# Performance work log

Hardware: AMD Instinct MI355X
Metric: run time of the kernel (lower is better)

The kernel has to match this reference:

```python
import jax, jax.numpy as jnp
import numpy as np

N = 131072      # total nodes = num_graphs * numNodes
E = 2097152     # edges (avg degree 16)
C_IN = 64
HID = 64        # hiddenChannels
NODES = 128     # numNodes per graph
B = 1024        # num_graphs
NCLS = 4


def setup_inputs() -> dict:
    key = jax.random.key(0)
    ks = jax.random.split(key, 10)
    x = jax.random.normal(ks[0], (N, C_IN), jnp.float32)
    edge_index = jax.random.randint(ks[1], (2, E), 0, N, dtype=jnp.int32)
    edge_attr = jax.random.uniform(ks[2], (E,), jnp.float32)
    # GCNConv params (stored as [in, out]); PyG uses glorot init, bias zeros
    W1 = jax.random.normal(ks[3], (C_IN, 2 * HID), jnp.float32) * (1.0 / np.sqrt(C_IN))
    b1 = jnp.zeros((2 * HID,), jnp.float32)
    W2 = jax.random.normal(ks[4], (2 * HID, HID), jnp.float32) * (1.0 / np.sqrt(2 * HID))
    b2 = jnp.zeros((HID,), jnp.float32)
    Wfc = jax.random.normal(ks[5], (HID * NODES, NCLS), jnp.float32) * (1.0 / np.sqrt(HID * NODES))
    bfc = jnp.zeros((NCLS,), jnp.float32)
    return {"x": x, "edge_index": edge_index, "edge_attr": edge_attr,
            "W1": W1, "b1": b1, "W2": W2, "b2": b2, "Wfc": Wfc, "bfc": bfc}


def gcn_conv(x, src, dst, ew, W, b):
    # PyG GCNConv: add self-loops (weight 1), symmetric normalization,
    # linear transform, scatter-add aggregation at target nodes, + bias.
    loop = jnp.arange(N, dtype=src.dtype)
    s = jnp.concatenate([src, loop])
    d = jnp.concatenate([dst, loop])
    w = jnp.concatenate([ew, jnp.ones((N,), ew.dtype)])
    deg = jax.ops.segment_sum(w, d, num_segments=N)                  # [N]
    dis = jnp.where(deg > 0, jax.lax.rsqrt(jnp.maximum(deg, 1e-30)), 0.0)
    norm = dis[s] * w * dis[d]                                       # [E+N]
    h = x @ W                                                        # [N, out]
    msg = h[s] * norm[:, None]                                       # gather + scale
    out = jax.ops.segment_sum(msg, d, num_segments=N)                # scatter-add
    return out + b


def reference(x, edge_index, edge_attr, W1, b1, W2, b2, Wfc, bfc):
    src, dst = edge_index[0], edge_index[1]
    h = jax.nn.relu(gcn_conv(x, src, dst, edge_attr, W1, b1))
    h = jax.nn.relu(gcn_conv(h, src, dst, edge_attr, W2, b2))
    h = h.reshape(B, HID * NODES)
    logits = h @ Wfc + bfc
    return jax.nn.softmax(logits, axis=1)
```

## Files before the change

kernel.cpp:

```cpp
#include <hip/hip_runtime.h>

#define N_NODES 131072
#define NE      2097152
#define CIN     64
#define HID     64
#define H2X     128
#define NODESG  128
#define NGRAPH  1024
#define NCLS    4

#define NBUCK   256
#define NPB     512
#define HBLK    1024
#define EPB     2048
#define DEGSC   1048576.0f
#define DEGMASK ((1ull << 40) - 1)

typedef short bf16x8 __attribute__((ext_vector_type(8)));
typedef float f32x4  __attribute__((ext_vector_type(4)));

__device__ __forceinline__ unsigned short f2b(float f) {
    unsigned int u = __float_as_uint(f);
    return (unsigned short)((u + 0x7fffu + ((u >> 16) & 1u)) >> 16);
}
__device__ __forceinline__ unsigned int pack2(float a, float b) {
    return (unsigned int)f2b(a) | ((unsigned int)f2b(b) << 16);
}
__device__ __forceinline__ float blo(unsigned u) { return __uint_as_float(u << 16); }
__device__ __forceinline__ float bhi(unsigned u) { return __uint_as_float(u & 0xffff0000u); }


__global__ __launch_bounds__(256) void k_wswiz(
        const float* __restrict__ W1, const float* __restrict__ W2,
        unsigned short* __restrict__ wf1, unsigned short* __restrict__ wf2) {
    int tid = threadIdx.x;
    #pragma unroll
    for (int it = 0; it < 4; ++it) {
        int idx = tid + 256 * it;
        int kt = idx >> 9, nt = (idx >> 6) & 7, l = idx & 63;
        int lm = l & 15, lq = l >> 4;
        unsigned pk[4];
        #pragma unroll
        for (int jp = 0; jp < 4; ++jp) {
            float w0 = W1[(kt*32 + lq*8 + 2*jp)     * H2X + nt*16 + lm];
            float w1 = W1[(kt*32 + lq*8 + 2*jp + 1) * H2X + nt*16 + lm];
            pk[jp] = pack2(w0, w1);
        }
        *(uint4*)&wf1[idx * 8] = make_uint4(pk[0], pk[1], pk[2], pk[3]);
    }
    #pragma unroll
    for (int it = 0; it < 4; ++it) {
        int idx = tid + 256 * it;
        int kt = idx >> 8, nt = (idx >> 6) & 3, l = idx & 63;
        int lm = l & 15, lq = l >> 4;
        unsigned pk[4];
        #pragma unroll
        for (int jp = 0; jp < 4; ++jp) {
            float w0 = W2[(kt*32 + lq*8 + 2*jp)     * HID + nt*16 + lm];
            float w1 = W2[(kt*32 + lq*8 + 2*jp + 1) * HID + nt*16 + lm];
            pk[jp] = pack2(w0, w1);
        }
        *(uint4*)&wf2[idx * 8] = make_uint4(pk[0], pk[1], pk[2], pk[3]);
    }
}


__global__ __launch_bounds__(256) void k_hist(const int* __restrict__ dst,
                                              int* __restrict__ hist) {
    __shared__ unsigned bh[NBUCK];
    int t = threadIdx.x;
    bh[t] = 0;
    __syncthreads();
    int base = blockIdx.x * EPB;
    #pragma unroll
    for (int k = 0; k < EPB / 256; ++k) {
        int d = dst[base + t + 256 * k];
        atomicAdd(&bh[d >> 9], 1u);
    }
    __syncthreads();
    hist[t * HBLK + blockIdx.x] = (int)bh[t];
}

__global__ void k_scan1(const int* __restrict__ in, int* __restrict__ out,
                        int* __restrict__ partial) {
    __shared__ int sd[256];
    int t = threadIdx.x;
    int base = blockIdx.x * 512;
    int c0 = in[base + 2*t];
    int c1 = in[base + 2*t + 1];
    int loc = c0 + c1;
    sd[t] = loc;
    __syncthreads();
    for (int off = 1; off < 256; off <<= 1) {
        int v = (t >= off) ? sd[t - off] : 0;
        __syncthreads();
        sd[t] += v;
        __syncthreads();
    }
    int excl = sd[t] - loc;
    out[base + 2*t]     = excl;
    out[base + 2*t + 1] = excl + c0;
    if (t == 255) partial[blockIdx.x] = sd[t];
}

__global__ void k_scan2(int* __restrict__ partial) {
    __shared__ int sd[256];
    int t = threadIdx.x;
    int p0 = partial[2*t], p1 = partial[2*t + 1];
    int loc = p0 + p1;
    sd[t] = loc;
    __syncthreads();
    for (int off = 1; off < 256; off <<= 1) {
        int v = (t >= off) ? sd[t - off] : 0;
        __syncthreads();
        sd[t] += v;
        __syncthreads();
    }
    int excl = sd[t] - loc;
    partial[2*t]     = excl;
    partial[2*t + 1] = excl + p0;
}

__global__ __launch_bounds__(256) void k_scatter(
        const int* __restrict__ src, const int* __restrict__ dst,
        const float* __restrict__ ew, const int* __restrict__ hist,
        const int* __restrict__ partial, unsigned long long* __restrict__ part) {
    __shared__ unsigned lcur[NBUCK];
    int t = threadIdx.x;
    int gi = t * HBLK + blockIdx.x;
    lcur[t] = (unsigned)(hist[gi] + partial[gi >> 9]);
    __syncthreads();
    int base = blockIdx.x * EPB;
    #pragma unroll
    for (int k = 0; k < EPB / 256; ++k) {
        int e = base + t + 256 * k;
        int s = src[e], d = dst[e];
        unsigned w = __float_as_uint(ew[e]);
        unsigned p = atomicAdd(&lcur[d >> 9], 1u);
        part[p] = ((unsigned long long)w << 32) |
                  ((unsigned long long)(unsigned)(d & 511) << 17) |
                  (unsigned long long)(unsigned)s;
    }
}

__global__ __launch_bounds__(256) void k_bucket(
        const unsigned long long* __restrict__ part, const int* __restrict__ hist,
        const int* __restrict__ partial, int2* __restrict__ csr,
        int* __restrict__ rowptr, int* __restrict__ counts, float* __restrict__ dis) {
    __shared__ unsigned long long dc[NPB];
    __shared__ unsigned cnt2[NPB];
    __shared__ int rp[NPB];
    __shared__ int sd[256];
    int t = threadIdx.x, b = blockIdx.x;
    dc[t] = 0; dc[t + 256] = 0;
    cnt2[t] = 0; cnt2[t + 256] = 0;
    __syncthreads();
    int start = hist[b * HBLK] + partial[2 * b];
    int end   = (b == NBUCK - 1) ? NE : (hist[(b + 1) * HBLK] + partial[2 * (b + 1)]);

    for (int j = start + t; j < end; j += 256) {
        unsigned long long p = part[j];
        unsigned dl = (unsigned)(p >> 17) & 511u;
        float w = __uint_as_float((unsigned)(p >> 32));
        atomicAdd(&dc[dl], (1ull << 40) | (unsigned long long)(unsigned)(w * DEGSC));
    }
    __syncthreads();

    unsigned long long d0 = dc[2*t], d1 = dc[2*t + 1];
    int c0 = (int)(d0 >> 40), c1 = (int)(d1 >> 40);
    int loc = c0 + c1;
    sd[t] = loc;
    __syncthreads();
    for (int off = 1; off < 256; off <<= 1) {
        int v = (t >= off) ? sd[t - off] : 0;
        __syncthreads();
        sd[t] += v;
        __syncthreads();
    }
    int excl = sd[t] - loc;
    rp[2*t] = excl; rp[2*t + 1] = excl + c0;

    int n0 = b * NPB;
    rowptr[n0 + 2*t]     = start + excl;
    rowptr[n0 + 2*t + 1] = start + excl + c0;
    counts[n0 + 2*t]     = c0;
    counts[n0 + 2*t + 1] = c1;
    float dg0 = (float)(d0 & DEGMASK) * (1.0f / DEGSC);
    float dg1 = (float)(d1 & DEGMASK) * (1.0f / DEGSC);
    dis[n0 + 2*t]     = rsqrtf(dg0 + 1.0f);
    dis[n0 + 2*t + 1] = rsqrtf(dg1 + 1.0f);
    __syncthreads();

    for (int j = start + t; j < end; j += 256) {
        unsigned long long p = part[j];
        unsigned dl = (unsigned)(p >> 17) & 511u;
        int s = (int)(p & 0x1ffffu);
        unsigned r = atomicAdd(&cnt2[dl], 1u);
        csr[start + rp[dl] + (int)r] = make_int2(s, (int)(unsigned)(p >> 32));
    }
}

__global__ void k_xcast(const float* __restrict__ x, const float* __restrict__ dis,
                        uint2* __restrict__ xb2) {
    int i = blockIdx.x * blockDim.x + threadIdx.x;
    float d = dis[i >> 4];
    float4 v = ((const float4*)x)[i];
    xb2[i] = make_uint2(pack2(d * v.x, d * v.y), pack2(d * v.z, d * v.w));
}


#define GATHER_PAIR(TAB, pA, pB, nA, nB, cmA, cmB, a0,a1,a2,a3, b0,b1,b2,b3, vSA, vSB) \
    {                                                                                  \
        int   sA0 = __shfl(pA.x, qid),      sA1 = __shfl(pA.x, qid + 4);               \
        int   sA2 = __shfl(pA.x, qid + 8),  sA3 = __shfl(pA.x, qid + 12);              \
        float fA0 = __int_as_float(__shfl(pA.y, qid));                                 \
        float fA1 = __int_as_float(__shfl(pA.y, qid + 4));                             \
        float fA2 = __int_as_float(__shfl(pA.y, qid + 8));                             \
        float fA3 = __int_as_float(__shfl(pA.y, qid + 12));                            \
        int   sB0 = __shfl(pB.x, qid),      sB1 = __shfl(pB.x, qid + 4);               \
        int   sB2 = __shfl(pB.x, qid + 8),  sB3 = __shfl(pB.x, qid + 12);              \
        float fB0 = __int_as_float(__shfl(pB.y, qid));                                 \
        float fB1 = __int_as_float(__shfl(pB.y, qid + 4));                             \
        float fB2 = __int_as_float(__shfl(pB.y, qid + 8));                             \
        float fB3 = __int_as_float(__shfl(pB.y, qid + 12));                            \
        uint2 vA0 = TAB[((unsigned)sA0 << 4) | ql];                                    \
        uint2 vA1 = TAB[((unsigned)sA1 << 4) | ql];                                    \
        uint2 vA2 = TAB[((unsigned)sA2 << 4) | ql];                                    \
        uint2 vA3 = TAB[((unsigned)sA3 << 4) | ql];                                    \
        uint2 vB0 = TAB[((unsigned)sB0 << 4) | ql];                                    \
        uint2 vB1 = TAB[((unsigned)sB1 << 4) | ql];                                    \
        uint2 vB2 = TAB[((unsigned)sB2 << 4) | ql];                                    \
        uint2 vB3 = TAB[((unsigned)sB3 << 4) | ql];                                    \
        vSA = TAB[((unsigned)nA << 4) | ql];                                           \
        vSB = TAB[((unsigned)nB << 4) | ql];                                           \
        a0 = fmaf(fA0, blo(vA0.x), a0); a1 = fmaf(fA0, bhi(vA0.x), a1);                \
        a2 = fmaf(fA0, blo(vA0.y), a2); a3 = fmaf(fA0, bhi(vA0.y), a3);                \
        a0 = fmaf(fA1, blo(vA1.x), a0); a1 = fmaf(fA1, bhi(vA1.x), a1);                \
        a2 = fmaf(fA1, blo(vA1.y), a2); a3 = fmaf(fA1, bhi(vA1.y), a3);                \
        a0 = fmaf(fA2, blo(vA2.x), a0); a1 = fmaf(fA2, bhi(vA2.x), a1);                \
        a2 = fmaf(fA2, blo(vA2.y), a2); a3 = fmaf(fA2, bhi(vA2.y), a3);                \
        a0 = fmaf(fA3, blo(vA3.x), a0); a1 = fmaf(fA3, bhi(vA3.x), a1);                \
        a2 = fmaf(fA3, blo(vA3.y), a2); a3 = fmaf(fA3, bhi(vA3.y), a3);                \
        b0 = fmaf(fB0, blo(vB0.x), b0); b1 = fmaf(fB0, bhi(vB0.x), b1);                \
        b2 = fmaf(fB0, blo(vB0.y), b2); b3 = fmaf(fB0, bhi(vB0.y), b3);                \
        b0 = fmaf(fB1, blo(vB1.x), b0); b1 = fmaf(fB1, bhi(vB1.x), b1);                \
        b2 = fmaf(fB1, blo(vB1.y), b2); b3 = fmaf(fB1, bhi(vB1.y), b3);                \
        b0 = fmaf(fB2, blo(vB2.x), b0); b1 = fmaf(fB2, bhi(vB2.x), b1);                \
        b2 = fmaf(fB2, blo(vB2.y), b2); b3 = fmaf(fB2, bhi(vB2.y), b3);                \
        b0 = fmaf(fB3, blo(vB3.x), b0); b1 = fmaf(fB3, bhi(vB3.x), b1);                \
        b2 = fmaf(fB3, blo(vB3.y), b2); b3 = fmaf(fB3, bhi(vB3.y), b3);                \
        int tsA = (cmA > 16) ? ((cmA - 13) >> 2) : 0;                                  \
        for (int k = 0; k < tsA; ++k) {                                                \
            int jj = 16 + 4 * k + qid;                                                 \
            int   s = __shfl(pA.x, jj);                                                \
            float f = __int_as_float(__shfl(pA.y, jj));                                \
            uint2 v = TAB[((unsigned)s << 4) | ql];                                    \
            a0 = fmaf(f, blo(v.x), a0); a1 = fmaf(f, bhi(v.x), a1);                    \
            a2 = fmaf(f, blo(v.y), a2); a3 = fmaf(f, bhi(v.y), a3);                    \
        }                                                                              \
        int tsB = (cmB > 16) ? ((cmB - 13) >> 2) : 0;                                  \
        for (int k = 0; k < tsB; ++k) {                                                \
            int jj = 16 + 4 * k + qid;                                                 \
            int   s = __shfl(pB.x, jj);                                                \
            float f = __int_as_float(__shfl(pB.y, jj));                                \
            uint2 v = TAB[((unsigned)s << 4) | ql];                                    \
            b0 = fmaf(f, blo(v.x), b0); b1 = fmaf(f, bhi(v.x), b1);                    \
            b2 = fmaf(f, blo(v.y), b2); b3 = fmaf(f, bhi(v.y), b3);                    \
        }                                                                              \
        a0 += __shfl_xor(a0, 16); a1 += __shfl_xor(a1, 16);                            \
        a2 += __shfl_xor(a2, 16); a3 += __shfl_xor(a3, 16);                            \
        a0 += __shfl_xor(a0, 32); a1 += __shfl_xor(a1, 32);                            \
        a2 += __shfl_xor(a2, 32); a3 += __shfl_xor(a3, 32);                            \
        b0 += __shfl_xor(b0, 16); b1 += __shfl_xor(b1, 16);                            \
        b2 += __shfl_xor(b2, 16); b3 += __shfl_xor(b3, 16);                            \
        b0 += __shfl_xor(b0, 32); b1 += __shfl_xor(b1, 32);                            \
        b2 += __shfl_xor(b2, 32); b3 += __shfl_xor(b3, 32);                            \
    }


__global__ __launch_bounds__(256, 4) void k_layer1(
        const uint2* __restrict__ xb2, const int2* __restrict__ csr,
        const int* __restrict__ rowptr, const int* __restrict__ counts,
        const float* __restrict__ dis, const unsigned short* __restrict__ wf1,
        const unsigned short* __restrict__ wf2, const float* __restrict__ b1,
        unsigned short* __restrict__ t2u) {
    __shared__ unsigned short sagg_b[32][72];
    __shared__ unsigned short sh1[32][136];
    __shared__ float sb[H2X];
    int tid = threadIdx.x;
    if (tid < H2X) sb[tid] = b1[tid];

    int wave = tid >> 6, lane = tid & 63;
    int qid = lane >> 4, ql = lane & 15;
    int n0 = blockIdx.x * 32;
    int nb = n0 + wave * 8;

    int cm8[8], cnt8[8], rs8[8];
    float dn8[8];
    int2 myp[8];
    #pragma unroll
    for (int i = 0; i < 8; ++i) {
        rs8[i] = rowptr[nb + i];
        cnt8[i] = counts[nb + i];
        dn8[i] = dis[nb + i];
        cm8[i] = cnt8[i] < 64 ? cnt8[i] : 64;
    }
    #pragma unroll
    for (int i = 0; i < 8; ++i)
        myp[i] = (lane < cm8[i]) ? csr[rs8[i] + lane] : make_int2(0, 0);

    #pragma unroll
    for (int ip = 0; ip < 8; ip += 2) {
        int2 pA = myp[ip], pB = myp[ip + 1];
        int nA = nb + ip, nB = nA + 1;
        float a0 = 0.f, a1 = 0.f, a2 = 0.f, a3 = 0.f;
        float b0 = 0.f, b1v = 0.f, b2v = 0.f, b3 = 0.f;
        uint2 vSA, vSB;
        GATHER_PAIR(xb2, pA, pB, nA, nB, cm8[ip], cm8[ip + 1],
                    a0, a1, a2, a3, b0, b1v, b2v, b3, vSA, vSB);
        for (int jj = 64; jj < cnt8[ip]; ++jj) {
            int2 p = csr[rs8[ip] + jj];
            float f = __int_as_float(p.y);
            uint2 v = xb2[((unsigned)p.x << 4) | ql];
            if (qid == 0) {
                a0 += f * blo(v.x); a1 += f * bhi(v.x);
                a2 += f * blo(v.y); a3 += f * bhi(v.y);
            }
        }
        for (int jj = 64; jj < cnt8[ip + 1]; ++jj) {
            int2 p = csr[rs8[ip + 1] + jj];
            float f = __int_as_float(p.y);
            uint2 v = xb2[((unsigned)p.x << 4) | ql];
            if (qid == 0) {
                b0 += f * blo(v.x); b1v += f * bhi(v.x);
                b2v += f * blo(v.y); b3 += f * bhi(v.y);
            }
        }
        if (qid == 0) {
            float dnA = dn8[ip], dnB = dn8[ip + 1];
            int m = wave * 8 + ip;
            *(uint2*)&sagg_b[m][ql * 4] =
                make_uint2(pack2(dnA * (a0 + blo(vSA.x)), dnA * (a1 + bhi(vSA.x))),
                           pack2(dnA * (a2 + blo(vSA.y)), dnA * (a3 + bhi(vSA.y))));
            *(uint2*)&sagg_b[m + 1][ql * 4] =
                make_uint2(pack2(dnB * (b0 + blo(vSB.x)), dnB * (b1v + bhi(vSB.x))),
                           pack2(dnB * (b2v + blo(vSB.y)), dnB * (b3 + bhi(vSB.y))));
        }
    }
    __syncthreads();

    int mt = wave & 1, ntb = (wave >> 1) * 4;
    int lm = lane & 15, lq = lane >> 4;
    bf16x8 af0 = *(const bf16x8*)&sagg_b[mt*16 + lm][lq * 8];
    bf16x8 af1 = *(const bf16x8*)&sagg_b[mt*16 + lm][32 + lq * 8];
    #pragma unroll
    for (int t = 0; t < 4; ++t) {
        int nt = ntb + t;
        bf16x8 bf0 = *(const bf16x8*)&wf1[(nt*64 + lane) * 8];
        bf16x8 bf1 = *(const bf16x8*)&wf1[((8 + nt)*64 + lane) * 8];
        f32x4 acc = {0.f, 0.f, 0.f, 0.f};
        acc = __builtin_amdgcn_mfma_f32_16x16x32_bf16(af0, bf0, acc, 0, 0, 0);
        acc = __builtin_amdgcn_mfma_f32_16x16x32_bf16(af1, bf1, acc, 0, 0, 0);
        int ch = nt*16 + lm;
        float bias = sb[ch];
        #pragma unroll
        for (int r = 0; r < 4; ++r)
            sh1[mt*16 + lq*4 + r][ch] = f2b(fmaxf(acc[r] + bias, 0.f));
    }
    __syncthreads();

    #pragma unroll
    for (int ti = 0; ti < 2; ++ti) {
        int t = wave * 2 + ti;
        int mt2 = t & 1, nt2 = t >> 1;
        f32x4 acc = {0.f, 0.f, 0.f, 0.f};
        #pragma unroll
        for (int kt = 0; kt < 4; ++kt) {
            bf16x8 af = *(const bf16x8*)&sh1[mt2*16 + lm][kt*32 + lq*8];
            bf16x8 bf = *(const bf16x8*)&wf2[((kt*4 + nt2)*64 + lane) * 8];
            acc = __builtin_amdgcn_mfma_f32_16x16x32_bf16(af, bf, acc, 0, 0, 0);
        }
        int ch = nt2*16 + lm;
        #pragma unroll
        for (int r = 0; r < 4; ++r) {
            int node = n0 + mt2*16 + lq*4 + r;
            t2u[(size_t)node * HID + ch] = f2b(dis[node] * acc[r]);
        }
    }
}


__global__ __launch_bounds__(256, 4) void k_agg2(
        const uint2* __restrict__ t2y, const int2* __restrict__ csr,
        const int* __restrict__ rowptr, const int* __restrict__ counts,
        const float* __restrict__ dis, const float* __restrict__ b2,
        unsigned short* __restrict__ h2b) {
    int tid = threadIdx.x;
    int wave = tid >> 6, lane = tid & 63;
    int qid = lane >> 4, ql = lane & 15;
    float4 bb = *(const float4*)&b2[ql * 4];
    int n0 = blockIdx.x * 32;
    int nb = n0 + wave * 8;

    int cm8[8], cnt8[8], rs8[8];
    float dn8[8];
    int2 myp[8];
    #pragma unroll
    for (int i = 0; i < 8; ++i) {
        rs8[i] = rowptr[nb + i];
        cnt8[i] = counts[nb + i];
        dn8[i] = dis[nb + i];
        cm8[i] = cnt8[i] < 64 ? cnt8[i] : 64;
    }
    #pragma unroll
    for (int i = 0; i < 8; ++i)
        myp[i] = (lane < cm8[i]) ? csr[rs8[i] + lane] : make_int2(0, 0);

    #pragma unroll
    for (int ip = 0; ip < 8; ip += 2) {
        int2 pA = myp[ip], pB = myp[ip + 1];
        int nA = nb + ip, nB = nA + 1;
        float a0 = 0.f, a1 = 0.f, a2 = 0.f, a3 = 0.f;
        float b0 = 0.f, b1v = 0.f, b2v = 0.f, b3 = 0.f;
        uint2 vSA, vSB;
        GATHER_PAIR(t2y, pA, pB, nA, nB, cm8[ip], cm8[ip + 1],
                    a0, a1, a2, a3, b0, b1v, b2v, b3, vSA, vSB);
        for (int jj = 64; jj < cnt8[ip]; ++jj) {
            int2 p = csr[rs8[ip] + jj];
            float f = __int_as_float(p.y);
            uint2 v = t2y[((unsigned)p.x << 4) | ql];
            if (qid == 0) {
                a0 += f * blo(v.x); a1 += f * bhi(v.x);
                a2 += f * blo(v.y); a3 += f * bhi(v.y);
            }
        }
        for (int jj = 64; jj < cnt8[ip + 1]; ++jj) {
            int2 p = csr[rs8[ip + 1] + jj];
            float f = __int_as_float(p.y);
            uint2 v = t2y[((unsigned)p.x << 4) | ql];
            if (qid == 0) {
                b0 += f * blo(v.x); b1v += f * bhi(v.x);
                b2v += f * blo(v.y); b3 += f * bhi(v.y);
            }
        }
        if (qid == 0) {
            float dnA = dn8[ip], dnB = dn8[ip + 1];
            float oa0 = fmaxf(fmaf(dnA, a0 + blo(vSA.x), bb.x), 0.f);
            float oa1 = fmaxf(fmaf(dnA, a1 + bhi(vSA.x), bb.y), 0.f);
            float oa2 = fmaxf(fmaf(dnA, a2 + blo(vSA.y), bb.z), 0.f);
            float oa3 = fmaxf(fmaf(dnA, a3 + bhi(vSA.y), bb.w), 0.f);
            float ob0 = fmaxf(fmaf(dnB, b0 + blo(vSB.x), bb.x), 0.f);
            float ob1 = fmaxf(fmaf(dnB, b1v + bhi(vSB.x), bb.y), 0.f);
            float ob2 = fmaxf(fmaf(dnB, b2v + blo(vSB.y), bb.z), 0.f);
            float ob3 = fmaxf(fmaf(dnB, b3 + bhi(vSB.y), bb.w), 0.f);
            *(uint2*)&h2b[((unsigned)nA << 6) | (ql * 4)] =
                make_uint2(pack2(oa0, oa1), pack2(oa2, oa3));
            *(uint2*)&h2b[((unsigned)nB << 6) | (ql * 4)] =
                make_uint2(pack2(ob0, ob1), pack2(ob2, ob3));
        }
    }
}


__global__ __launch_bounds__(256) void k_fc(
        const unsigned short* __restrict__ h2b, const float* __restrict__ Wfc,
        const float* __restrict__ bfc, float* __restrict__ out) {
    __shared__ float4 red[256];
    int b = blockIdx.x, t = threadIdx.x;
    const uint2* hrow = (const uint2*)(h2b + (size_t)b * (HID * NODESG));
    const float4* W4 = (const float4*)Wfc;
    float4 a = make_float4(0.f, 0.f, 0.f, 0.f);
    #pragma unroll
    for (int j = 0; j < 8; ++j) {
        int i = j * 256 + t;
        uint2 hv = hrow[i];
        float h0 = blo(hv.x), h1 = bhi(hv.x), h2v = blo(hv.y), h3 = bhi(hv.y);
        float4 w0 = W4[i * 4 + 0];
        float4 w1 = W4[i * 4 + 1];
        float4 w2 = W4[i * 4 + 2];
        float4 w3 = W4[i * 4 + 3];
        a.x = fmaf(h0, w0.x, a.x); a.y = fmaf(h0, w0.y, a.y);
        a.z = fmaf(h0, w0.z, a.z); a.w = fmaf(h0, w0.w, a.w);
        a.x = fmaf(h1, w1.x, a.x); a.y = fmaf(h1, w1.y, a.y);
        a.z = fmaf(h1, w1.z, a.z); a.w = fmaf(h1, w1.w, a.w);
        a.x = fmaf(h2v, w2.x, a.x); a.y = fmaf(h2v, w2.y, a.y);
        a.z = fmaf(h2v, w2.z, a.z); a.w = fmaf(h2v, w2.w, a.w);
        a.x = fmaf(h3, w3.x, a.x); a.y = fmaf(h3, w3.y, a.y);
        a.z = fmaf(h3, w3.z, a.z); a.w = fmaf(h3, w3.w, a.w);
    }
    red[t] = a;
    __syncthreads();
    for (int s = 128; s > 0; s >>= 1) {
        if (t < s) {
            red[t].x += red[t + s].x; red[t].y += red[t + s].y;
            red[t].z += red[t + s].z; red[t].w += red[t + s].w;
        }
        __syncthreads();
    }
    if (t == 0) {
        float l0 = red[0].x + bfc[0];
        float l1 = red[0].y + bfc[1];
        float l2 = red[0].z + bfc[2];
        float l3 = red[0].w + bfc[3];
        float mx = fmaxf(fmaxf(l0, l1), fmaxf(l2, l3));
        float e0 = expf(l0 - mx), e1 = expf(l1 - mx);
        float e2 = expf(l2 - mx), e3 = expf(l3 - mx);
        float inv = 1.f / (e0 + e1 + e2 + e3);
        float4 o = make_float4(e0 * inv, e1 * inv, e2 * inv, e3 * inv);
        *(float4*)&out[(size_t)b * 4] = o;
    }
}


extern "C" void kernel_launch(void* const* d_in, const int* in_sizes, int n_in,
                              void* d_out, int out_size, void* d_ws, size_t ws_size,
                              hipStream_t stream) {
    const float* x   = (const float*)d_in[0];
    const int*   ei  = (const int*)  d_in[1];
    const float* ea  = (const float*)d_in[2];
    const float* W1  = (const float*)d_in[3];
    const float* b1  = (const float*)d_in[4];
    const float* W2  = (const float*)d_in[5];
    const float* b2  = (const float*)d_in[6];
    const float* Wfc = (const float*)d_in[7];
    const float* bfc = (const float*)d_in[8];
    float* out = (float*)d_out;
    const int* src = ei;
    const int* dst = ei + NE;

    char* ws = (char*)d_ws;
    size_t off = 0;
    int*   hist   = (int*)  (ws + off); off += (size_t)NBUCK * HBLK * 4;
    int*   partial= (int*)  (ws + off); off += 4096;
    int*   counts = (int*)  (ws + off); off += (size_t)N_NODES * 4;
    int*   rowptr = (int*)  (ws + off); off += (size_t)N_NODES * 4;
    float* dis    = (float*)(ws + off); off += (size_t)N_NODES * 4;
    unsigned short* wf1 = (unsigned short*)(ws + off); off += 8192 * 2;
    unsigned short* wf2 = (unsigned short*)(ws + off); off += 8192 * 2;
    int2*  csr    = (int2*) (ws + off); off += (size_t)NE * 8;
    uint2* xb2    = (uint2*)(ws + off); off += (size_t)N_NODES * CIN * 2;
    unsigned short* t2u = (unsigned short*)(ws + off); off += (size_t)N_NODES * HID * 2;
    unsigned short* h2b = (unsigned short*)(ws + off); off += (size_t)N_NODES * HID * 2;
    unsigned long long* part = (unsigned long long*)t2u;

    hipMemsetAsync(hist, 0, (size_t)NBUCK * HBLK * 4 + 4096, stream);

    k_wswiz  <<<1, 256, 0, stream>>>(W1, W2, wf1, wf2);
    k_hist   <<<HBLK, 256, 0, stream>>>(dst, hist);
    k_scan1  <<<NBUCK * HBLK / 512, 256, 0, stream>>>(hist, hist, partial);
    k_scan2  <<<1, 256, 0, stream>>>(partial);
    k_scatter<<<HBLK, 256, 0, stream>>>(src, dst, ea, hist, partial, part);
    k_bucket <<<NBUCK, 256, 0, stream>>>(part, hist, partial, csr, rowptr, counts, dis);
    k_xcast  <<<(N_NODES * CIN / 4) / 256, 256, 0, stream>>>(x, dis, xb2);
    k_layer1 <<<N_NODES / 32, 256, 0, stream>>>(xb2, csr, rowptr, counts, dis,
                                                wf1, wf2, b1, t2u);
    k_agg2   <<<N_NODES / 32, 256, 0, stream>>>((const uint2*)t2u, csr, rowptr,
                                                counts, dis, b2, h2b);
    k_fc     <<<NGRAPH, 256, 0, stream>>>(h2b, Wfc, bfc, out);
}
```

Baseline: 264.2 us.

## Use 1024 finer buckets in CSR build, parallelize weight swizzle, drop memset

The counting-sort CSR construction now uses 1024 buckets of 128 nodes instead of 256 buckets of 512 nodes. This gives the bucket kernel four times as many blocks with smaller shared-memory work, and the histogram, scatter and scan kernels are adapted to match. The weight swizzle runs on 8 blocks instead of one, and the workspace memset is removed because every hist entry is written anyway. In exchange the histogram and scan arrays grow four times larger, and the per-block scans inside the bucket kernel leave most threads idle.

```diff
diff --git a/kernel.cpp b/kernel.cpp
--- a/kernel.cpp
+++ b/kernel.cpp
@@ -9,8 +9,8 @@
 #define NGRAPH  1024
 #define NCLS    4
 
-#define NBUCK   256
-#define NPB     512
+#define NBUCK   1024
+#define NPB     128
 #define HBLK    1024
 #define EPB     2048
 #define DEGSC   1048576.0f
@@ -33,10 +33,8 @@
 __global__ __launch_bounds__(256) void k_wswiz(
         const float* __restrict__ W1, const float* __restrict__ W2,
         unsigned short* __restrict__ wf1, unsigned short* __restrict__ wf2) {
-    int tid = threadIdx.x;
-    #pragma unroll
-    for (int it = 0; it < 4; ++it) {
-        int idx = tid + 256 * it;
+    int idx = blockIdx.x * 256 + threadIdx.x;
+    if (idx < 1024) {
         int kt = idx >> 9, nt = (idx >> 6) & 7, l = idx & 63;
         int lm = l & 15, lq = l >> 4;
         unsigned pk[4];
@@ -47,11 +45,9 @@
             pk[jp] = pack2(w0, w1);
         }
         *(uint4*)&wf1[idx * 8] = make_uint4(pk[0], pk[1], pk[2], pk[3]);
-    }
-    #pragma unroll
-    for (int it = 0; it < 4; ++it) {
-        int idx = tid + 256 * it;
-        int kt = idx >> 8, nt = (idx >> 6) & 3, l = idx & 63;
+    } else {
+        int j = idx - 1024;
+        int kt = j >> 8, nt = (j >> 6) & 3, l = j & 63;
         int lm = l & 15, lq = l >> 4;
         unsigned pk[4];
         #pragma unroll
@@ -60,7 +56,7 @@
             float w1 = W2[(kt*32 + lq*8 + 2*jp + 1) * HID + nt*16 + lm];
             pk[jp] = pack2(w0, w1);
         }
-        *(uint4*)&wf2[idx * 8] = make_uint4(pk[0], pk[1], pk[2], pk[3]);
+        *(uint4*)&wf2[j * 8] = make_uint4(pk[0], pk[1], pk[2], pk[3]);
     }
 }
 
@@ -69,16 +65,21 @@
                                               int* __restrict__ hist) {
     __shared__ unsigned bh[NBUCK];
     int t = threadIdx.x;
-    bh[t] = 0;
+    #pragma unroll
+    for (int k = 0; k < NBUCK / 256; ++k) bh[t + 256 * k] = 0;
     __syncthreads();
     int base = blockIdx.x * EPB;
     #pragma unroll
     for (int k = 0; k < EPB / 256; ++k) {
         int d = dst[base + t + 256 * k];
-        atomicAdd(&bh[d >> 9], 1u);
-    }
-    __syncthreads();
-    hist[t * HBLK + blockIdx.x] = (int)bh[t];
+        atomicAdd(&bh[d >> 7], 1u);
+    }
+    __syncthreads();
+    #pragma unroll
+    for (int k = 0; k < NBUCK / 256; ++k) {
+        int b4 = t + 256 * k;
+        hist[b4 * HBLK + blockIdx.x] = (int)bh[b4];
+    }
 }
 
 __global__ void k_scan1(const int* __restrict__ in, int* __restrict__ out,
@@ -106,19 +107,20 @@
 __global__ void k_scan2(int* __restrict__ partial) {
     __shared__ int sd[256];
     int t = threadIdx.x;
-    int p0 = partial[2*t], p1 = partial[2*t + 1];
-    int loc = p0 + p1;
+    int v[8]; int loc = 0;
+    #pragma unroll
+    for (int i = 0; i < 8; ++i) { v[i] = partial[t * 8 + i]; loc += v[i]; }
     sd[t] = loc;
     __syncthreads();
     for (int off = 1; off < 256; off <<= 1) {
-        int v = (t >= off) ? sd[t - off] : 0;
-        __syncthreads();
-        sd[t] += v;
+        int vv = (t >= off) ? sd[t - off] : 0;
+        __syncthreads();
+        sd[t] += vv;
         __syncthreads();
     }
     int excl = sd[t] - loc;
-    partial[2*t]     = excl;
-    partial[2*t + 1] = excl + p0;
+    #pragma unroll
+    for (int i = 0; i < 8; ++i) { partial[t * 8 + i] = excl; excl += v[i]; }
 }
 
 __global__ __launch_bounds__(256) void k_scatter(
@@ -127,8 +129,12 @@
         const int* __restrict__ partial, unsigned long long* __restrict__ part) {
     __shared__ unsigned lcur[NBUCK];
     int t = threadIdx.x;
-    int gi = t * HBLK + blockIdx.x;
-    lcur[t] = (unsigned)(hist[gi] + partial[gi >> 9]);
+    #pragma unroll
+    for (int k = 0; k < NBUCK / 256; ++k) {
+        int b4 = t + 256 * k;
+        int gi = b4 * HBLK + blockIdx.x;
+        lcur[b4] = (unsigned)(hist[gi] + partial[gi >> 9]);
+    }
     __syncthreads();
     int base = blockIdx.x * EPB;
     #pragma unroll
@@ -136,9 +142,9 @@
         int e = base + t + 256 * k;
         int s = src[e], d = dst[e];
         unsigned w = __float_as_uint(ew[e]);
-        unsigned p = atomicAdd(&lcur[d >> 9], 1u);
+        unsigned p = atomicAdd(&lcur[d >> 7], 1u);
         part[p] = ((unsigned long long)w << 32) |
-                  ((unsigned long long)(unsigned)(d & 511) << 17) |
+                  ((unsigned long long)(unsigned)(d & 127) << 17) |
                   (unsigned long long)(unsigned)s;
     }
 }
@@ -150,50 +156,54 @@
     __shared__ unsigned long long dc[NPB];
     __shared__ unsigned cnt2[NPB];
     __shared__ int rp[NPB];
-    __shared__ int sd[256];
+    __shared__ int sd[64];
     int t = threadIdx.x, b = blockIdx.x;
-    dc[t] = 0; dc[t + 256] = 0;
-    cnt2[t] = 0; cnt2[t + 256] = 0;
+    if (t < NPB) { dc[t] = 0; cnt2[t] = 0; }
     __syncthreads();
     int start = hist[b * HBLK] + partial[2 * b];
     int end   = (b == NBUCK - 1) ? NE : (hist[(b + 1) * HBLK] + partial[2 * (b + 1)]);
 
     for (int j = start + t; j < end; j += 256) {
         unsigned long long p = part[j];
-        unsigned dl = (unsigned)(p >> 17) & 511u;
+        unsigned dl = (unsigned)(p >> 17) & 127u;
         float w = __uint_as_float((unsigned)(p >> 32));
         atomicAdd(&dc[dl], (1ull << 40) | (unsigned long long)(unsigned)(w * DEGSC));
     }
     __syncthreads();
 
-    unsigned long long d0 = dc[2*t], d1 = dc[2*t + 1];
-    int c0 = (int)(d0 >> 40), c1 = (int)(d1 >> 40);
-    int loc = c0 + c1;
-    sd[t] = loc;
-    __syncthreads();
-    for (int off = 1; off < 256; off <<= 1) {
-        int v = (t >= off) ? sd[t - off] : 0;
-        __syncthreads();
-        sd[t] += v;
-        __syncthreads();
-    }
-    int excl = sd[t] - loc;
-    rp[2*t] = excl; rp[2*t + 1] = excl + c0;
-
-    int n0 = b * NPB;
-    rowptr[n0 + 2*t]     = start + excl;
-    rowptr[n0 + 2*t + 1] = start + excl + c0;
-    counts[n0 + 2*t]     = c0;
-    counts[n0 + 2*t + 1] = c1;
-    float dg0 = (float)(d0 & DEGMASK) * (1.0f / DEGSC);
-    float dg1 = (float)(d1 & DEGMASK) * (1.0f / DEGSC);
-    dis[n0 + 2*t]     = rsqrtf(dg0 + 1.0f);
-    dis[n0 + 2*t + 1] = rsqrtf(dg1 + 1.0f);
+    int c0 = 0, c1 = 0, loc = 0;
+    unsigned long long d0 = 0, d1 = 0;
+    if (t < 64) {
+        d0 = dc[2*t]; d1 = dc[2*t + 1];
+        c0 = (int)(d0 >> 40); c1 = (int)(d1 >> 40);
+        loc = c0 + c1;
+        sd[t] = loc;
+    }
+    __syncthreads();
+    for (int off = 1; off < 64; off <<= 1) {
+        int v = (t < 64 && t >= off) ? sd[t - off] : 0;
+        __syncthreads();
+        if (t < 64) sd[t] += v;
+        __syncthreads();
+    }
+    if (t < 64) {
+        int excl = sd[t] - loc;
+        rp[2*t] = excl; rp[2*t + 1] = excl + c0;
+        int n0 = b * NPB;
+        rowptr[n0 + 2*t]     = start + excl;
+        rowptr[n0 + 2*t + 1] = start + excl + c0;
+        counts[n0 + 2*t]     = c0;
+        counts[n0 + 2*t + 1] = c1;
+        float dg0 = (float)(d0 & DEGMASK) * (1.0f / DEGSC);
+        float dg1 = (float)(d1 & DEGMASK) * (1.0f / DEGSC);
+        dis[n0 + 2*t]     = rsqrtf(dg0 + 1.0f);
+        dis[n0 + 2*t + 1] = rsqrtf(dg1 + 1.0f);
+    }
     __syncthreads();
 
     for (int j = start + t; j < end; j += 256) {
         unsigned long long p = part[j];
-        unsigned dl = (unsigned)(p >> 17) & 511u;
+        unsigned dl = (unsigned)(p >> 17) & 127u;
         int s = (int)(p & 0x1ffffu);
         unsigned r = atomicAdd(&cnt2[dl], 1u);
         csr[start + rp[dl] + (int)r] = make_int2(s, (int)(unsigned)(p >> 32));
@@ -531,7 +541,7 @@
     char* ws = (char*)d_ws;
     size_t off = 0;
     int*   hist   = (int*)  (ws + off); off += (size_t)NBUCK * HBLK * 4;
-    int*   partial= (int*)  (ws + off); off += 4096;
+    int*   partial= (int*)  (ws + off); off += 8192;
     int*   counts = (int*)  (ws + off); off += (size_t)N_NODES * 4;
     int*   rowptr = (int*)  (ws + off); off += (size_t)N_NODES * 4;
     float* dis    = (float*)(ws + off); off += (size_t)N_NODES * 4;
@@ -543,9 +553,8 @@
     unsigned short* h2b = (unsigned short*)(ws + off); off += (size_t)N_NODES * HID * 2;
     unsigned long long* part = (unsigned long long*)t2u;
 
-    hipMemsetAsync(hist, 0, (size_t)NBUCK * HBLK * 4 + 4096, stream);
-
-    k_wswiz  <<<1, 256, 0, stream>>>(W1, W2, wf1, wf2);
+
+    k_wswiz  <<<8, 256, 0, stream>>>(W1, W2, wf1, wf2);
     k_hist   <<<HBLK, 256, 0, stream>>>(dst, hist);
     k_scan1  <<<NBUCK * HBLK / 512, 256, 0, stream>>>(hist, hist, partial);
     k_scan2  <<<1, 256, 0, stream>>>(partial);
```

After: 273.3 us. +3.4%, slower.
